# Optimization experiments

Hardware: AMD Instinct MI355X
Metric: run time of the kernel (lower is better)

The kernel has to match this reference:

```python
import jax, jax.numpy as jnp
import numpy as np

B, N, D = 4, 2048, 1024
H, A, Lv = 8, 128, 128   # heads, attention_dim (qk), linear_dim (v)
NUM_BLOCKS = 4
QKV_W = (2 * Lv + 2 * A) * H  # 4096
NEG = -1e9


def setup_inputs() -> dict:
    key = jax.random.key(0)
    ks = jax.random.split(key, 10)
    past_lengths = jax.random.randint(ks[0], (B,), 0, N)
    past_ids = jax.random.randint(ks[1], (B, N), 0, 10000)
    past_embeddings = jax.random.normal(ks[2], (B, N, D), dtype=jnp.float32)
    # per-block parameters, stacked on leading block axis (xavier-ish scale)
    qkv_w = jax.random.normal(ks[3], (NUM_BLOCKS, D, QKV_W), dtype=jnp.float32) * (1.0 / np.sqrt(D))
    qkv_b = jnp.zeros((NUM_BLOCKS, QKV_W), dtype=jnp.float32)
    out_w = jax.random.normal(ks[4], (NUM_BLOCKS, Lv * H, D), dtype=jnp.float32) * (1.0 / np.sqrt(Lv * H))
    out_b = jnp.zeros((NUM_BLOCKS, D), dtype=jnp.float32)
    ln_g = jnp.ones((NUM_BLOCKS, D), dtype=jnp.float32)
    ln_b = jnp.zeros((NUM_BLOCKS, D), dtype=jnp.float32)
    return {"past_lengths": past_lengths, "past_ids": past_ids,
            "past_embeddings": past_embeddings, "qkv_w": qkv_w, "qkv_b": qkv_b,
            "out_w": out_w, "out_b": out_b, "ln_g": ln_g, "ln_b": ln_b}


def _layer_norm(x, g, b, eps=1e-5):
    mu = jnp.mean(x, axis=-1, keepdims=True)
    var = jnp.mean(jnp.square(x - mu), axis=-1, keepdims=True)
    return (x - mu) * jax.lax.rsqrt(var + eps) * g + b


def _block(x, mask, qw, qb, ow, ob, g, b):
    xn = _layer_norm(x, g, b)
    qkv = (xn @ qw + qb).reshape(B, N, H, 2 * Lv + 2 * A)
    q = qkv[..., :A]              # [B,N,H,A]
    k = qkv[..., A:2 * A]         # [B,N,H,A]
    v = qkv[..., 2 * A:2 * A + Lv]  # [B,N,H,Lv]
    scores = jnp.einsum('bnha,bmha->bhnm', q, k) / np.sqrt(A)
    # original: masked_fill(-inf) -> silu -> /N -> softmax; we mask after the
    # silu transform with a large-negative logit so masked weights are ~0
    logits = jnp.where(mask[:, None, :, :], jax.nn.silu(scores) / N, NEG)
    w = jax.nn.softmax(logits, axis=-1)
    attn = jnp.einsum('bhnm,bmhl->bnhl', w, v).reshape(B, N, H * Lv)
    return x + attn @ ow + ob


def reference(past_lengths, past_ids, past_embeddings, qkv_w, qkv_b, out_w, out_b, ln_g, ln_b):
    valid = past_ids != 0                                   # [B,N]
    causal = jnp.triu(jnp.ones((N, N), dtype=bool), k=1)     # faithful to buffer (triu, diag=1)
    mask = causal[None] & valid[:, None, :] & valid[:, :, None]  # [B,N,N]
    x = past_embeddings
    for i in range(NUM_BLOCKS):
        x = _block(x, mask, qkv_w[i], qkv_b[i], out_w[i], out_b[i], ln_g[i], ln_b[i])
    return x
```

## Files before the change

### kernel.cpp

```cpp
#include <hip/hip_runtime.h>

typedef __bf16 bf16_t;
typedef __bf16 bf16x8 __attribute__((ext_vector_type(8)));
typedef __bf16 bf16x4 __attribute__((ext_vector_type(4)));
typedef float f32x4 __attribute__((ext_vector_type(4)));
typedef unsigned int u32x4 __attribute__((ext_vector_type(4)));

#define B_ 4
#define N_ 2048
#define D_ 1024
#define H_ 8
#define NB_ 4
#define M_ (B_*N_)
#define QN_ 3072
#define QKN_ 2048

__device__ __forceinline__ void async_copy16(const void* gsrc, void* ldst) {
    __builtin_amdgcn_global_load_lds(
        (const __attribute__((address_space(1))) void*)gsrc,
        (__attribute__((address_space(3))) void*)ldst, 16, 0, 0);
}

static constexpr size_t WT_OFF  = 0;
static constexpr size_t WT_SZ   = (size_t)NB_*QN_*D_*2;
static constexpr size_t OWT_OFF = WT_OFF + WT_SZ;
static constexpr size_t OWT_SZ  = (size_t)NB_*D_*D_*2;
static constexpr size_t XN_OFF  = OWT_OFF + OWT_SZ;
static constexpr size_t XN_SZ   = (size_t)M_*D_*2;
static constexpr size_t QK_OFF  = XN_OFF + XN_SZ;
static constexpr size_t QK_SZ   = (size_t)M_*QKN_*2;
static constexpr size_t VT_OFF  = QK_OFF + QK_SZ;
static constexpr size_t VT_SZ   = (size_t)32*128*N_*2;
static constexpr size_t ATT_OFF = VT_OFF + VT_SZ;
static constexpr size_t ATT_SZ  = (size_t)M_*D_*2;
static constexpr size_t QBR_OFF = ATT_OFF + ATT_SZ;
static constexpr size_t QBR_SZ  = (size_t)NB_*QN_*4;
static constexpr size_t VS_OFF  = QBR_OFF + QBR_SZ;
static constexpr size_t VS_SZ   = (size_t)32*128*4;
static constexpr size_t MASK_OFF = VS_OFF + VS_SZ;

__global__ __launch_bounds__(256) void repack_qkvw(const float* __restrict__ qw, bf16_t* __restrict__ wt)
{
    __shared__ float tile[64][65];
    const int nb = blockIdx.z;
    const int j0 = blockIdx.x * 64, d0 = blockIdx.y * 64;
    const int tx = threadIdx.x, ty = threadIdx.y;
    const float* src = qw + (size_t)nb * D_ * 4096;
    const int jj = j0 + tx;
    const int sel = jj >> 10, rr = jj & 1023, hh = rr >> 7, aa = rr & 127;
    const int orig = hh * 512 + sel * 128 + aa;
#pragma unroll
    for (int it = 0; it < 16; ++it) {
        int dr = it * 4 + ty;
        tile[dr][tx] = src[(size_t)(d0 + dr) * 4096 + orig];
    }
    __syncthreads();
    bf16_t* dst = wt + (size_t)nb * QN_ * D_;
#pragma unroll
    for (int it = 0; it < 16; ++it) {
        int jr = it * 4 + ty;
        dst[(size_t)(j0 + jr) * D_ + d0 + tx] = (bf16_t)tile[tx][jr];
    }
}

__global__ __launch_bounds__(256) void repack_outw(const float* __restrict__ ow, bf16_t* __restrict__ owt)
{
    __shared__ float tile[64][65];
    const int nb = blockIdx.z;
    const int j0 = blockIdx.x * 64, d0 = blockIdx.y * 64;
    const int tx = threadIdx.x, ty = threadIdx.y;
    const float* src = ow + (size_t)nb * D_ * D_;
#pragma unroll
    for (int it = 0; it < 16; ++it) {
        int dr = it * 4 + ty;
        tile[dr][tx] = src[(size_t)(d0 + dr) * D_ + j0 + tx];
    }
    __syncthreads();
    bf16_t* dst = owt + (size_t)nb * D_ * D_;
#pragma unroll
    for (int it = 0; it < 16; ++it) {
        int jr = it * 4 + ty;
        dst[(size_t)(j0 + jr) * D_ + d0 + tx] = (bf16_t)tile[tx][jr];
    }
}

__global__ __launch_bounds__(256) void repack_qb(const float* __restrict__ qb, float* __restrict__ qbr)
{
    int idx = blockIdx.x * 256 + threadIdx.x;
    int nb = idx / QN_, jj = idx % QN_;
    int sel = jj >> 10, rr = jj & 1023, hh = rr >> 7, aa = rr & 127;
    qbr[idx] = qb[nb * 4096 + hh * 512 + sel * 128 + aa];
}

__global__ __launch_bounds__(256) void mask_kernel(const int* __restrict__ past_ids, unsigned short* __restrict__ maskA)
{
    const int idx = blockIdx.x * 256 + threadIdx.x;
    const int b = idx >> 11, P = idx & 2047;
    const int k = P & 31;
    const int m = (P & ~31) | (((k >> 2) & 1) << 4) | (((k >> 3) & 3) << 2) | (k & 3);
    maskA[idx] = past_ids[b * N_ + m] != 0 ? 0xFFFFu : 0u;
}

__global__ __launch_bounds__(256) void ln_kernel(const float* __restrict__ x, const float* __restrict__ g,
                                                 const float* __restrict__ bb, bf16_t* __restrict__ xn)
{
    const int row = blockIdx.x, tid = threadIdx.x;
    const float4 v = ((const float4*)(x + (size_t)row * D_))[tid];
    float s = v.x + v.y + v.z + v.w;
    float q = v.x * v.x + v.y * v.y + v.z * v.z + v.w * v.w;
#pragma unroll
    for (int d = 32; d >= 1; d >>= 1) { s += __shfl_xor(s, d); q += __shfl_xor(q, d); }
    __shared__ float ls[4], lq[4];
    if ((tid & 63) == 0) { ls[tid >> 6] = s; lq[tid >> 6] = q; }
    __syncthreads();
    s = ls[0] + ls[1] + ls[2] + ls[3];
    q = lq[0] + lq[1] + lq[2] + lq[3];
    const float mean = s * (1.f / 1024.f);
    const float var  = q * (1.f / 1024.f) - mean * mean;
    const float inv  = rsqrtf(var + 1e-5f);
    const float4 gg = ((const float4*)g)[tid];
    const float4 bv = ((const float4*)bb)[tid];
    bf16x4 o;
    o[0] = (bf16_t)((v.x - mean) * inv * gg.x + bv.x);
    o[1] = (bf16_t)((v.y - mean) * inv * gg.y + bv.y);
    o[2] = (bf16_t)((v.z - mean) * inv * gg.z + bv.z);
    o[3] = (bf16_t)((v.w - mean) * inv * gg.w + bv.w);
    *(bf16x4*)(xn + (size_t)row * D_ + tid * 4) = o;
}

__global__ __launch_bounds__(512, 2) void gemm_qkv(const bf16_t* __restrict__ Am, const bf16_t* __restrict__ Bt,
                                                   const float* __restrict__ bias,
                                                   bf16_t* __restrict__ outQK, bf16_t* __restrict__ vtOut)
{
    __shared__ bf16_t As[4 * 8192];
    __shared__ bf16_t Bs[4 * 6144];
    const int tid = threadIdx.x;
    const int lane = tid & 63, wave = tid >> 6;
    const int wr = wave >> 2, wc = wave & 3;
    const int quad = lane >> 4, l15 = lane & 15;
    const int swz = quad ^ ((l15 >> 1) & 3);
    const int slane8 = ((lane & 3) ^ ((lane >> 3) & 3)) * 8;
    const int lrow = lane >> 2;
    const int m0 = blockIdx.y * 256, n0 = blockIdx.x * 192;
    const int Kn = D_;
    const bool w4 = (wave < 4);

    const int ch = wave * 2;
    const int bch0 = w4 ? 2 * wave : 4 + wave;
    const int bch1 = w4 ? 2 * wave + 1 : bch0;
    const bf16_t* gA0 = Am + (size_t)(m0 + ch * 16 + lrow) * Kn + slane8;
    const bf16_t* gA1 = gA0 + (size_t)16 * Kn;
    const bf16_t* gB0 = Bt + (size_t)(n0 + bch0 * 16 + lrow) * Kn + slane8;
    const bf16_t* gB1 = Bt + (size_t)(n0 + bch1 * 16 + lrow) * Kn + slane8;
    bf16_t* const dA0 = &As[ch * 512 + lane * 8];
    bf16_t* const dA1 = &As[(ch + 1) * 512 + lane * 8];
    bf16_t* const dB0 = &Bs[bch0 * 512 + lane * 8];
    bf16_t* const dB1 = &Bs[bch1 * 512 + lane * 8];

    auto STAGE = [&](int slot) {
        async_copy16(gA0, dA0 + slot * 8192);
        async_copy16(gA1, dA1 + slot * 8192);
        async_copy16(gB0, dB0 + slot * 6144);
        if (w4) async_copy16(gB1, dB1 + slot * 6144);
        gA0 += 32; gA1 += 32; gB0 += 32; gB1 += 32;
    };

    f32x4 acc[8][3] = {};
    const int NT = Kn >> 5;

    STAGE(0); STAGE(1); STAGE(2);
    if (w4) asm volatile("s_waitcnt vmcnt(8)" ::: "memory");
    else    asm volatile("s_waitcnt vmcnt(6)" ::: "memory");
    __builtin_amdgcn_s_barrier();

    const int aoff = wr * 4096 + l15 * 32 + swz * 8;
    const int boff = wc * 1536 + l15 * 32 + swz * 8;

    for (int t = 0; t < NT; ++t) {
        const int ring = t & 3;
        const bf16_t* ra = &As[ring * 8192 + aoff];
        const bf16_t* rb = &Bs[ring * 6144 + boff];
        bf16x8 af[8], bfv[3];
#pragma unroll
        for (int j = 0; j < 3; ++j) bfv[j] = *(const bf16x8*)(rb + j * 512);
#pragma unroll
        for (int i = 0; i < 8; ++i) af[i] = *(const bf16x8*)(ra + i * 512);
        if (t + 3 < NT) STAGE((t + 3) & 3);
        __builtin_amdgcn_s_setprio(1);
#pragma unroll
        for (int i = 0; i < 8; ++i)
#pragma unroll
            for (int j = 0; j < 3; ++j)
                acc[i][j] = __builtin_amdgcn_mfma_f32_16x16x32_bf16(af[i], bfv[j], acc[i][j], 0, 0, 0);
        __builtin_amdgcn_s_setprio(0);
        if (t + 3 < NT) {
            if (w4) asm volatile("s_waitcnt vmcnt(8)" ::: "memory");
            else    asm volatile("s_waitcnt vmcnt(6)" ::: "memory");
        } else if (t + 2 < NT) {
            if (w4) asm volatile("s_waitcnt vmcnt(4)" ::: "memory");
            else    asm volatile("s_waitcnt vmcnt(3)" ::: "memory");
        } else if (t + 1 < NT) {
            asm volatile("s_waitcnt vmcnt(0)" ::: "memory");
        }
        __builtin_amdgcn_s_barrier();
    }

#pragma unroll
    for (int i = 0; i < 8; ++i) {
        const int rowg = m0 + wr * 128 + i * 16 + quad * 4;
        const int bb2 = rowg >> 11, mloc = rowg & 2047;
        const int mperm = (mloc & ~31) | (((mloc >> 2) & 3) << 3) | (((mloc >> 4) & 1) << 2);
#pragma unroll
        for (int j = 0; j < 3; ++j) {
            const int colg = n0 + wc * 48 + j * 16 + l15;
            const float bv = bias[colg];
            if (colg >= 2048) {
                const int hh = (colg - 2048) >> 7, ll = (colg - 2048) & 127;
                bf16x4 sv;
#pragma unroll
                for (int r = 0; r < 4; ++r) sv[r] = (bf16_t)(acc[i][j][r] + bv);
                *(bf16x4*)(vtOut + ((size_t)(bb2 * 8 + hh) * 128 + ll) * (size_t)N_ + mperm) = sv;
            } else {
                const float qs = (colg < 1024) ? 0.08838834764831845f : 1.f;
#pragma unroll
                for (int r = 0; r < 4; ++r)
                    outQK[(size_t)(rowg + r) * QKN_ + colg] = (bf16_t)((acc[i][j][r] + bv) * qs);
            }
        }
    }
}

template<bool RESID>
__global__ __launch_bounds__(512, 2) void gemm256(const bf16_t* __restrict__ Am, const bf16_t* __restrict__ Bt,
                                                  const float* __restrict__ bias, float* __restrict__ resid_out,
                                                  bf16_t* __restrict__ outH, bf16_t* __restrict__ vtOut,
                                                  int Kn, int Nn, int vSplit)
{
    __shared__ bf16_t As[4 * 256 * 32];
    __shared__ bf16_t Bs[4 * 128 * 32];
    const int tid = threadIdx.x;
    const int lane = tid & 63, wave = tid >> 6;
    const int wr = wave >> 2, wc = wave & 3;
    const int quad = lane >> 4, l15 = lane & 15;
    const int swz = quad ^ ((l15 >> 1) & 3);
    const int slane8 = ((lane & 3) ^ ((lane >> 3) & 3)) * 8;
    const int lrow = lane >> 2;
    const int m0 = blockIdx.y * 256, n0 = blockIdx.x * 128;

    const int chA0 = wave * 2, chA1 = chA0 + 1;
    const bf16_t* gA0 = Am + (size_t)(m0 + chA0 * 16 + lrow) * Kn + slane8;
    const bf16_t* gA1 = Am + (size_t)(m0 + chA1 * 16 + lrow) * Kn + slane8;
    const bf16_t* gB  = Bt + (size_t)(n0 + wave * 16 + lrow) * Kn + slane8;
    bf16_t* const dA0 = &As[chA0 * 512];
    bf16_t* const dA1 = &As[chA1 * 512];
    bf16_t* const dB  = &Bs[wave * 512];

    auto STAGE = [&](int slot) {
        async_copy16(gA0, dA0 + slot * 8192);
        async_copy16(gA1, dA1 + slot * 8192);
        async_copy16(gB,  dB  + slot * 4096);
        gA0 += 32; gA1 += 32; gB += 32;
    };

    f32x4 acc[8][2] = {};
    const int NT = Kn >> 5;

    STAGE(0); STAGE(1); STAGE(2);
    asm volatile("s_waitcnt vmcnt(6)" ::: "memory");
    __builtin_amdgcn_s_barrier();

    const int aoff = (wr * 128 + l15) * 32 + swz * 8;
    const int boff = (wc * 32  + l15) * 32 + swz * 8;

    for (int t = 0; t < NT; ++t) {
        const int ring = t & 3;
        const bf16_t* ra = &As[ring * 8192 + aoff];
        const bf16_t* rb = &Bs[ring * 4096 + boff];
        bf16x8 af[8], bfv[2];
#pragma unroll
        for (int i = 0; i < 8; ++i) af[i] = *(const bf16x8*)(ra + i * 512);
#pragma unroll
        for (int j = 0; j < 2; ++j) bfv[j] = *(const bf16x8*)(rb + j * 512);
        if (t + 3 < NT) STAGE((t + 3) & 3);
        __builtin_amdgcn_s_barrier();
        asm volatile("s_waitcnt lgkmcnt(0)" ::: "memory");
        __builtin_amdgcn_s_setprio(1);
#pragma unroll
        for (int i = 0; i < 8; ++i)
#pragma unroll
            for (int j = 0; j < 2; ++j)
                acc[i][j] = __builtin_amdgcn_mfma_f32_16x16x32_bf16(af[i], bfv[j], acc[i][j], 0, 0, 0);
        __builtin_amdgcn_s_setprio(0);
        if (t + 3 < NT)      asm volatile("s_waitcnt vmcnt(6)" ::: "memory");
        else if (t + 2 < NT) asm volatile("s_waitcnt vmcnt(3)" ::: "memory");
        else if (t + 1 < NT) asm volatile("s_waitcnt vmcnt(0)" ::: "memory");
        __builtin_amdgcn_s_barrier();
    }

    if (!RESID && n0 >= vSplit) {
#pragma unroll
        for (int i = 0; i < 8; ++i) {
            const int rowg = m0 + wr * 128 + i * 16 + quad * 4;
            const int bb2 = rowg >> 11, mloc = rowg & 2047;
            const int mperm = (mloc & ~31) | (((mloc >> 2) & 3) << 3) | (((mloc >> 4) & 1) << 2);
#pragma unroll
            for (int j = 0; j < 2; ++j) {
                const int colg = n0 + wc * 32 + j * 16 + l15;
                const int hh = (colg - 2048) >> 7, ll = (colg - 2048) & 127;
                const float bv = bias[colg];
                bf16x4 sv;
#pragma unroll
                for (int r = 0; r < 4; ++r) sv[r] = (bf16_t)(acc[i][j][r] + bv);
                *(bf16x4*)(vtOut + ((size_t)(bb2 * 8 + hh) * 128 + ll) * (size_t)N_ + mperm) = sv;
            }
        }
        return;
    }
#pragma unroll
    for (int i = 0; i < 8; ++i) {
#pragma unroll
        for (int j = 0; j < 2; ++j) {
            const int colg = n0 + wc * 32 + j * 16 + l15;
            const float bv = bias[colg];
#pragma unroll
            for (int r = 0; r < 4; ++r) {
                const int rowg = m0 + wr * 128 + i * 16 + quad * 4 + r;
                const size_t off = (size_t)rowg * Nn + colg;
                const float v = acc[i][j][r] + bv;
                if (RESID) resid_out[off] += v;
                else       outH[off] = (bf16_t)v;
            }
        }
    }
}

__global__ __launch_bounds__(256) void vsum_kernel(const bf16_t* __restrict__ vt, float* __restrict__ vs)
{
    const int gid = blockIdx.x * 4 + (threadIdx.x >> 6);
    const int lane = threadIdx.x & 63;
    const bf16_t* p = vt + (size_t)gid * N_ + lane * 8;
    float s = 0.f;
#pragma unroll
    for (int c = 0; c < 4; ++c) {
        bf16x8 v = *(const bf16x8*)(p + c * 512);
#pragma unroll
        for (int u = 0; u < 8; ++u) s += (float)v[u];
    }
#pragma unroll
    for (int d = 32; d >= 1; d >>= 1) s += __shfl_xor(s, d);
    if (lane == 0) vs[gid] = s;
}

template<bool CAUSAL>
__device__ __forceinline__ void attn_tile(
    int m0, int m0n, int n0, int b, int h,
    const bf16_t* __restrict__ qk, const bf16_t* __restrict__ vtb,
    const unsigned short* __restrict__ maskB,
    bf16_t* Ks, bf16_t* Vs,
    const bf16x8 (&qf)[2][4], bf16x8 onesf,
    f32x4 (&oacc)[2][8], f32x4 (&dacc)[2])
{
    const int tid = threadIdx.x, lane = tid & 63, wave = tid >> 6;
    const int quad = lane >> 4, l15 = lane & 15;
    const int swz = quad ^ ((l15 >> 1) & 3);
    const int slane8 = ((lane & 3) ^ ((lane >> 3) & 3)) * 8;
    const int lrow = lane >> 2;
    const float invN = 1.f / 2048.f;

#pragma unroll
    for (int s = 0; s < 8; ++s) {
        const int kkc = s & 3, rg = (s >> 2) + wave * 2;
        async_copy16(vtb + (size_t)(rg * 16 + lrow) * N_ + m0 + kkc * 32 + slane8,
                     &Vs[kkc * 4096 + rg * 512 + lane * 8]);
    }
    bf16x8 mAf[4];
#pragma unroll
    for (int kk = 0; kk < 4; ++kk)
        mAf[kk] = *(const bf16x8*)(maskB + m0 + kk * 32 + quad * 8);

    f32x4 sacc[2][8] = {};
    __builtin_amdgcn_s_setprio(1);
#pragma unroll
    for (int kk = 0; kk < 4; ++kk) {
#pragma unroll
        for (int j = 0; j < 8; ++j) {
            bf16x8 kf = *(const bf16x8*)&Ks[kk * 4096 + (j * 16 + l15) * 32 + swz * 8];
            sacc[0][j] = __builtin_amdgcn_mfma_f32_16x16x32_bf16(kf, qf[0][kk], sacc[0][j], 0, 0, 0);
            sacc[1][j] = __builtin_amdgcn_mfma_f32_16x16x32_bf16(kf, qf[1][kk], sacc[1][j], 0, 0, 0);
        }
    }
    __builtin_amdgcn_s_setprio(0);

    bf16x8 pf[2][4];
#pragma unroll
    for (int kk = 0; kk < 4; ++kk) {
#pragma unroll
        for (int s = 0; s < 2; ++s) {
            const int j = kk * 2 + s;
#pragma unroll
            for (int nb = 0; nb < 2; ++nb) {
#pragma unroll
                for (int r = 0; r < 4; ++r) {
                    const float sv = sacc[nb][j][r];
                    const float xc = __builtin_amdgcn_fmed3f(sv, -4.f, 4.f);
                    float sg = __builtin_fmaf(xc, 0.25f * invN, 0.5f * invN);
                    sg = __builtin_fmaf(-(xc * (0.03125f * invN)), fabsf(xc), sg);
                    float e = __builtin_fmaf(sv, sg, 1.f);
                    if (CAUSAL) {
                        const int dmn = (m0 + j * 16 + quad * 4 + r) - (n0 + wave * 32 + nb * 16 + l15);
                        e = (dmn > 0) ? e : 0.f;
                    }
                    pf[nb][kk][s * 4 + r] = (bf16_t)e;
                }
            }
        }
        *(u32x4*)&pf[0][kk] = *(u32x4*)&pf[0][kk] & *(const u32x4*)&mAf[kk];
        *(u32x4*)&pf[1][kk] = *(u32x4*)&pf[1][kk] & *(const u32x4*)&mAf[kk];
    }

    __syncthreads();

    if (m0n < N_) {
        const size_t baseq = (size_t)b * N_ * QKN_;
#pragma unroll
        for (int s = 0; s < 8; ++s) {
            const int kkc = s & 3, rg = (s >> 2) + wave * 2;
            async_copy16(qk + baseq + (size_t)(m0n + rg * 16 + lrow) * QKN_ + 1024 + h * 128 + kkc * 32 + slane8,
                         &Ks[kkc * 4096 + rg * 512 + lane * 8]);
        }
    }

    __builtin_amdgcn_s_setprio(1);
#pragma unroll
    for (int kk = 0; kk < 4; ++kk) {
        dacc[0] = __builtin_amdgcn_mfma_f32_16x16x32_bf16(pf[0][kk], onesf, dacc[0], 0, 0, 0);
        dacc[1] = __builtin_amdgcn_mfma_f32_16x16x32_bf16(pf[1][kk], onesf, dacc[1], 0, 0, 0);
#pragma unroll
        for (int j = 0; j < 8; ++j) {
            bf16x8 vf = *(const bf16x8*)&Vs[kk * 4096 + (j * 16 + l15) * 32 + swz * 8];
            oacc[0][j] = __builtin_amdgcn_mfma_f32_16x16x32_bf16(pf[0][kk], vf, oacc[0][j], 0, 0, 0);
            oacc[1][j] = __builtin_amdgcn_mfma_f32_16x16x32_bf16(pf[1][kk], vf, oacc[1][j], 0, 0, 0);
        }
    }
    __builtin_amdgcn_s_setprio(0);
    __syncthreads();
}

__global__ __launch_bounds__(256, 2) void attn_kernel(const bf16_t* __restrict__ qk, const bf16_t* __restrict__ vt,
                                                      const int* __restrict__ past_ids, const float* __restrict__ vsum,
                                                      const unsigned short* __restrict__ maskA,
                                                      bf16_t* __restrict__ att)
{
    __shared__ bf16_t Ks[4 * 128 * 32];
    __shared__ bf16_t Vs[4 * 128 * 32];

    const int bx = blockIdx.x;
    const int bh = bx & 31, g = bx >> 5;
    const int t = (g < 8) ? g : 23 - g;
    const int b = bh >> 3, h = bh & 7;
    const int n0 = t << 7;
    const int tid = threadIdx.x, lane = tid & 63, wave = tid >> 6;
    const int quad = lane >> 4, l15 = lane & 15;
    const int slane8 = ((lane & 3) ^ ((lane >> 3) & 3)) * 8;
    const int lrow = lane >> 2;
    const bf16_t* vtb = vt + (size_t)bh * 128 * N_;
    const unsigned short* maskB = maskA + b * N_;
    const float invN = 1.f / 2048.f;

    bf16x8 qf[2][4];
#pragma unroll
    for (int nb = 0; nb < 2; ++nb) {
        const bf16_t* gq = qk + (size_t)b * N_ * QKN_ + (size_t)(n0 + wave * 32 + nb * 16 + l15) * QKN_ + h * 128 + quad * 8;
#pragma unroll
        for (int kk = 0; kk < 4; ++kk) qf[nb][kk] = *(const bf16x8*)(gq + kk * 32);
    }
    const float vnf0 = past_ids[b * N_ + n0 + wave * 32 + l15] != 0 ? 1.f : 0.f;
    const float vnf1 = past_ids[b * N_ + n0 + wave * 32 + 16 + l15] != 0 ? 1.f : 0.f;
    bf16x8 onesf;
#pragma unroll
    for (int i = 0; i < 8; ++i) onesf[i] = (bf16_t)1.f;

    {
        const size_t baseq = (size_t)b * N_ * QKN_;
#pragma unroll
        for (int s = 0; s < 8; ++s) {
            const int kkc = s & 3, rg = (s >> 2) + wave * 2;
            async_copy16(qk + baseq + (size_t)(n0 + rg * 16 + lrow) * QKN_ + 1024 + h * 128 + kkc * 32 + slane8,
                         &Ks[kkc * 4096 + rg * 512 + lane * 8]);
        }
    }
    __syncthreads();

    f32x4 oacc[2][8] = {};
    f32x4 dacc[2] = {};

    attn_tile<true>(n0, n0 + 128, n0, b, h, qk, vtb, maskB, Ks, Vs, qf, onesf, oacc, dacc);
    for (int m0 = n0 + 128; m0 < N_; m0 += 128)
        attn_tile<false>(m0, m0 + 128, n0, b, h, qk, vtb, maskB, Ks, Vs, qf, onesf, oacc, dacc);

    float vsr[8];
#pragma unroll
    for (int j = 0; j < 8; ++j) vsr[j] = vsum[bh * 128 + j * 16 + l15];
#pragma unroll
    for (int nb = 0; nb < 2; ++nb) {
        const float vn = nb ? vnf1 : vnf0;
#pragma unroll
        for (int r = 0; r < 4; ++r) {
            const float dn = dacc[nb][r];
            const bool uni = (vn == 0.f) || !(dn > 0.f);
            const float rc = uni ? 0.f : __builtin_amdgcn_rcpf(dn);
            const int gn = n0 + wave * 32 + nb * 16 + quad * 4 + r;
#pragma unroll
            for (int j = 0; j < 8; ++j) {
                const float ov = uni ? (vsr[j] * invN) : (oacc[nb][j][r] * rc);
                att[(size_t)(b * N_ + gn) * 1024 + h * 128 + j * 16 + l15] = (bf16_t)ov;
            }
        }
    }
}

extern "C" void kernel_launch(void* const* d_in, const int* in_sizes, int n_in,
                              void* d_out, int out_size, void* d_ws, size_t ws_size,
                              hipStream_t stream) {
    (void)in_sizes; (void)n_in; (void)out_size; (void)ws_size;
    const int*   past_ids = (const int*)d_in[1];
    const float* past_emb = (const float*)d_in[2];
    const float* qkv_w    = (const float*)d_in[3];
    const float* qkv_b    = (const float*)d_in[4];
    const float* out_w    = (const float*)d_in[5];
    const float* out_b    = (const float*)d_in[6];
    const float* ln_g     = (const float*)d_in[7];
    const float* ln_b     = (const float*)d_in[8];

    float* x = (float*)d_out;
    char* ws = (char*)d_ws;
    bf16_t* WT  = (bf16_t*)(ws + WT_OFF);
    bf16_t* OWT = (bf16_t*)(ws + OWT_OFF);
    bf16_t* XN  = (bf16_t*)(ws + XN_OFF);
    bf16_t* QK  = (bf16_t*)(ws + QK_OFF);
    bf16_t* VT  = (bf16_t*)(ws + VT_OFF);
    bf16_t* ATT = (bf16_t*)(ws + ATT_OFF);
    float*  QBR = (float*)(ws + QBR_OFF);
    float*  VS  = (float*)(ws + VS_OFF);
    unsigned short* MASKA = (unsigned short*)(ws + MASK_OFF);

    hipMemcpyAsync(x, past_emb, (size_t)M_ * D_ * sizeof(float), hipMemcpyDeviceToDevice, stream);
    repack_qkvw<<<dim3(48, 16, NB_), dim3(64, 4), 0, stream>>>(qkv_w, WT);
    repack_outw<<<dim3(16, 16, NB_), dim3(64, 4), 0, stream>>>(out_w, OWT);
    repack_qb<<<48, 256, 0, stream>>>(qkv_b, QBR);
    mask_kernel<<<32, 256, 0, stream>>>(past_ids, MASKA);

    for (int layer = 0; layer < NB_; ++layer) {
        ln_kernel<<<M_, 256, 0, stream>>>(x, ln_g + layer * D_, ln_b + layer * D_, XN);
        gemm_qkv<<<dim3(QN_ / 192, M_ / 256), 512, 0, stream>>>(
            XN, WT + (size_t)layer * QN_ * D_, QBR + layer * QN_, QK, VT);
        vsum_kernel<<<1024, 256, 0, stream>>>(VT, VS);
        attn_kernel<<<512, 256, 0, stream>>>(QK, VT, past_ids, VS, MASKA, ATT);
        gemm256<true><<<dim3(D_ / 128, M_ / 256), 512, 0, stream>>>(
            ATT, OWT + (size_t)layer * D_ * D_, out_b + layer * D_, x, nullptr, nullptr, D_, D_, 1 << 30);
    }
}
```

Baseline: 868.6 us.

## Fuse V column sums into QKV GEMM epilogue and drop the initial residual copy

The per-head V row sums are now accumulated in the QKV GEMM epilogue with wave shuffles and atomicAdd into per-layer buffers that the mask kernel zeroes, so the separate vsum kernel is removed. The up-front device-to-device copy of the embeddings is gone: layer 0 reads past_emb directly and the output GEMM writes resid_in plus the projection instead of accumulating in place. The output GEMM also drops a barrier and an explicit LDS wait in its main loop, and changes how it computes its LDS staging addresses. The aim is to save one kernel launch per layer and one 32 MB copy, at the cost of float atomics whose summation order is nondeterministic.

```diff
diff --git a/kernel.cpp b/kernel.cpp
--- a/kernel.cpp
+++ b/kernel.cpp
@@ -36,7 +36,7 @@
 static constexpr size_t QBR_OFF = ATT_OFF + ATT_SZ;
 static constexpr size_t QBR_SZ  = (size_t)NB_*QN_*4;
 static constexpr size_t VS_OFF  = QBR_OFF + QBR_SZ;
-static constexpr size_t VS_SZ   = (size_t)32*128*4;
+static constexpr size_t VS_SZ   = (size_t)NB_*32*128*4;
 static constexpr size_t MASK_OFF = VS_OFF + VS_SZ;
 
 __global__ __launch_bounds__(256) void repack_qkvw(const float* __restrict__ qw, bf16_t* __restrict__ wt)
@@ -92,9 +92,11 @@
     qbr[idx] = qb[nb * 4096 + hh * 512 + sel * 128 + aa];
 }
 
-__global__ __launch_bounds__(256) void mask_kernel(const int* __restrict__ past_ids, unsigned short* __restrict__ maskA)
+__global__ __launch_bounds__(256) void mask_kernel(const int* __restrict__ past_ids, unsigned short* __restrict__ maskA,
+                                                   float* __restrict__ vsl)
 {
     const int idx = blockIdx.x * 256 + threadIdx.x;
+    vsl[idx] = 0.f; vsl[idx + 8192] = 0.f;
     const int b = idx >> 11, P = idx & 2047;
     const int k = P & 31;
     const int m = (P & ~31) | (((k >> 2) & 1) << 4) | (((k >> 3) & 3) << 2) | (k & 3);
@@ -130,7 +132,8 @@
 
 __global__ __launch_bounds__(512, 2) void gemm_qkv(const bf16_t* __restrict__ Am, const bf16_t* __restrict__ Bt,
                                                    const float* __restrict__ bias,
-                                                   bf16_t* __restrict__ outQK, bf16_t* __restrict__ vtOut)
+                                                   bf16_t* __restrict__ outQK, bf16_t* __restrict__ vtOut,
+                                                   float* __restrict__ vsOut)
 {
     __shared__ bf16_t As[4 * 8192];
     __shared__ bf16_t Bs[4 * 6144];
@@ -205,23 +208,32 @@
         __builtin_amdgcn_s_barrier();
     }
 
-#pragma unroll
-    for (int i = 0; i < 8; ++i) {
-        const int rowg = m0 + wr * 128 + i * 16 + quad * 4;
-        const int bb2 = rowg >> 11, mloc = rowg & 2047;
-        const int mperm = (mloc & ~31) | (((mloc >> 2) & 3) << 3) | (((mloc >> 4) & 1) << 2);
-#pragma unroll
-        for (int j = 0; j < 3; ++j) {
-            const int colg = n0 + wc * 48 + j * 16 + l15;
-            const float bv = bias[colg];
-            if (colg >= 2048) {
-                const int hh = (colg - 2048) >> 7, ll = (colg - 2048) & 127;
+    const int bb2 = m0 >> 11;
+#pragma unroll
+    for (int j = 0; j < 3; ++j) {
+        const int colg = n0 + wc * 48 + j * 16 + l15;
+        const float bv = bias[colg];
+        if (colg >= 2048) {
+            const int hh = (colg - 2048) >> 7, ll = (colg - 2048) & 127;
+            float ps = 32.f * bv;
+#pragma unroll
+            for (int i = 0; i < 8; ++i) {
+                const int rowg = m0 + wr * 128 + i * 16 + quad * 4;
+                const int mloc = rowg & 2047;
+                const int mperm = (mloc & ~31) | (((mloc >> 2) & 3) << 3) | (((mloc >> 4) & 1) << 2);
                 bf16x4 sv;
 #pragma unroll
-                for (int r = 0; r < 4; ++r) sv[r] = (bf16_t)(acc[i][j][r] + bv);
+                for (int r = 0; r < 4; ++r) { sv[r] = (bf16_t)(acc[i][j][r] + bv); ps += acc[i][j][r]; }
                 *(bf16x4*)(vtOut + ((size_t)(bb2 * 8 + hh) * 128 + ll) * (size_t)N_ + mperm) = sv;
-            } else {
-                const float qs = (colg < 1024) ? 0.08838834764831845f : 1.f;
+            }
+            ps += __shfl_xor(ps, 16);
+            ps += __shfl_xor(ps, 32);
+            if (quad == 0) atomicAdd(&vsOut[(size_t)(bb2 * 8 + hh) * 128 + ll], ps);
+        } else {
+            const float qs = (colg < 1024) ? 0.08838834764831845f : 1.f;
+#pragma unroll
+            for (int i = 0; i < 8; ++i) {
+                const int rowg = m0 + wr * 128 + i * 16 + quad * 4;
 #pragma unroll
                 for (int r = 0; r < 4; ++r)
                     outQK[(size_t)(rowg + r) * QKN_ + colg] = (bf16_t)((acc[i][j][r] + bv) * qs);
@@ -230,11 +242,9 @@
     }
 }
 
-template<bool RESID>
-__global__ __launch_bounds__(512, 2) void gemm256(const bf16_t* __restrict__ Am, const bf16_t* __restrict__ Bt,
-                                                  const float* __restrict__ bias, float* __restrict__ resid_out,
-                                                  bf16_t* __restrict__ outH, bf16_t* __restrict__ vtOut,
-                                                  int Kn, int Nn, int vSplit)
+__global__ __launch_bounds__(512, 2) void gemm_out(const bf16_t* __restrict__ Am, const bf16_t* __restrict__ Bt,
+                                                   const float* __restrict__ bias,
+                                                   const float* __restrict__ resid_in, float* __restrict__ resid_out)
 {
     __shared__ bf16_t As[4 * 256 * 32];
     __shared__ bf16_t Bs[4 * 128 * 32];
@@ -246,14 +256,15 @@
     const int slane8 = ((lane & 3) ^ ((lane >> 3) & 3)) * 8;
     const int lrow = lane >> 2;
     const int m0 = blockIdx.y * 256, n0 = blockIdx.x * 128;
+    const int Kn = D_;
 
     const int chA0 = wave * 2, chA1 = chA0 + 1;
     const bf16_t* gA0 = Am + (size_t)(m0 + chA0 * 16 + lrow) * Kn + slane8;
     const bf16_t* gA1 = Am + (size_t)(m0 + chA1 * 16 + lrow) * Kn + slane8;
     const bf16_t* gB  = Bt + (size_t)(n0 + wave * 16 + lrow) * Kn + slane8;
-    bf16_t* const dA0 = &As[chA0 * 512];
-    bf16_t* const dA1 = &As[chA1 * 512];
-    bf16_t* const dB  = &Bs[wave * 512];
+    bf16_t* const dA0 = &As[chA0 * 512 + lane * 8];
+    bf16_t* const dA1 = &As[chA1 * 512 + lane * 8];
+    bf16_t* const dB  = &Bs[wave * 512 + lane * 8];
 
     auto STAGE = [&](int slot) {
         async_copy16(gA0, dA0 + slot * 8192);
@@ -278,12 +289,10 @@
         const bf16_t* rb = &Bs[ring * 4096 + boff];
         bf16x8 af[8], bfv[2];
 #pragma unroll
+        for (int j = 0; j < 2; ++j) bfv[j] = *(const bf16x8*)(rb + j * 512);
+#pragma unroll
         for (int i = 0; i < 8; ++i) af[i] = *(const bf16x8*)(ra + i * 512);
-#pragma unroll
-        for (int j = 0; j < 2; ++j) bfv[j] = *(const bf16x8*)(rb + j * 512);
         if (t + 3 < NT) STAGE((t + 3) & 3);
-        __builtin_amdgcn_s_barrier();
-        asm volatile("s_waitcnt lgkmcnt(0)" ::: "memory");
         __builtin_amdgcn_s_setprio(1);
 #pragma unroll
         for (int i = 0; i < 8; ++i)
@@ -297,25 +306,6 @@
         __builtin_amdgcn_s_barrier();
     }
 
-    if (!RESID && n0 >= vSplit) {
-#pragma unroll
-        for (int i = 0; i < 8; ++i) {
-            const int rowg = m0 + wr * 128 + i * 16 + quad * 4;
-            const int bb2 = rowg >> 11, mloc = rowg & 2047;
-            const int mperm = (mloc & ~31) | (((mloc >> 2) & 3) << 3) | (((mloc >> 4) & 1) << 2);
-#pragma unroll
-            for (int j = 0; j < 2; ++j) {
-                const int colg = n0 + wc * 32 + j * 16 + l15;
-                const int hh = (colg - 2048) >> 7, ll = (colg - 2048) & 127;
-                const float bv = bias[colg];
-                bf16x4 sv;
-#pragma unroll
-                for (int r = 0; r < 4; ++r) sv[r] = (bf16_t)(acc[i][j][r] + bv);
-                *(bf16x4*)(vtOut + ((size_t)(bb2 * 8 + hh) * 128 + ll) * (size_t)N_ + mperm) = sv;
-            }
-        }
-        return;
-    }
 #pragma unroll
     for (int i = 0; i < 8; ++i) {
 #pragma unroll
@@ -325,30 +315,11 @@
 #pragma unroll
             for (int r = 0; r < 4; ++r) {
                 const int rowg = m0 + wr * 128 + i * 16 + quad * 4 + r;
-                const size_t off = (size_t)rowg * Nn + colg;
-                const float v = acc[i][j][r] + bv;
-                if (RESID) resid_out[off] += v;
-                else       outH[off] = (bf16_t)v;
+                const size_t off = (size_t)rowg * D_ + colg;
+                resid_out[off] = resid_in[off] + acc[i][j][r] + bv;
             }
         }
     }
-}
-
-__global__ __launch_bounds__(256) void vsum_kernel(const bf16_t* __restrict__ vt, float* __restrict__ vs)
-{
-    const int gid = blockIdx.x * 4 + (threadIdx.x >> 6);
-    const int lane = threadIdx.x & 63;
-    const bf16_t* p = vt + (size_t)gid * N_ + lane * 8;
-    float s = 0.f;
-#pragma unroll
-    for (int c = 0; c < 4; ++c) {
-        bf16x8 v = *(const bf16x8*)(p + c * 512);
-#pragma unroll
-        for (int u = 0; u < 8; ++u) s += (float)v[u];
-    }
-#pragma unroll
-    for (int d = 32; d >= 1; d >>= 1) s += __shfl_xor(s, d);
-    if (lane == 0) vs[gid] = s;
 }
 
 template<bool CAUSAL>
@@ -541,22 +512,21 @@
     bf16_t* VT  = (bf16_t*)(ws + VT_OFF);
     bf16_t* ATT = (bf16_t*)(ws + ATT_OFF);
     float*  QBR = (float*)(ws + QBR_OFF);
-    float*  VS  = (float*)(ws + VS_OFF);
+    float*  VSL = (float*)(ws + VS_OFF);
     unsigned short* MASKA = (unsigned short*)(ws + MASK_OFF);
 
-    hipMemcpyAsync(x, past_emb, (size_t)M_ * D_ * sizeof(float), hipMemcpyDeviceToDevice, stream);
     repack_qkvw<<<dim3(48, 16, NB_), dim3(64, 4), 0, stream>>>(qkv_w, WT);
     repack_outw<<<dim3(16, 16, NB_), dim3(64, 4), 0, stream>>>(out_w, OWT);
     repack_qb<<<48, 256, 0, stream>>>(qkv_b, QBR);
-    mask_kernel<<<32, 256, 0, stream>>>(past_ids, MASKA);
+    mask_kernel<<<32, 256, 0, stream>>>(past_ids, MASKA, VSL);
 
     for (int layer = 0; layer < NB_; ++layer) {
-        ln_kernel<<<M_, 256, 0, stream>>>(x, ln_g + layer * D_, ln_b + layer * D_, XN);
+        const float* xin = (layer == 0) ? past_emb : x;
+        ln_kernel<<<M_, 256, 0, stream>>>(xin, ln_g + layer * D_, ln_b + layer * D_, XN);
         gemm_qkv<<<dim3(QN_ / 192, M_ / 256), 512, 0, stream>>>(
-            XN, WT + (size_t)layer * QN_ * D_, QBR + layer * QN_, QK, VT);
-        vsum_kernel<<<1024, 256, 0, stream>>>(VT, VS);
-        attn_kernel<<<512, 256, 0, stream>>>(QK, VT, past_ids, VS, MASKA, ATT);
-        gemm256<true><<<dim3(D_ / 128, M_ / 256), 512, 0, stream>>>(
-            ATT, OWT + (size_t)layer * D_ * D_, out_b + layer * D_, x, nullptr, nullptr, D_, D_, 1 << 30);
-    }
-}
+            XN, WT + (size_t)layer * QN_ * D_, QBR + layer * QN_, QK, VT, VSL + layer * 4096);
+        attn_kernel<<<512, 256, 0, stream>>>(QK, VT, past_ids, VSL + layer * 4096, MASKA, ATT);
+        gemm_out<<<dim3(D_ / 128, M_ / 256), 512, 0, stream>>>(
+            ATT, OWT + (size_t)layer * D_ * D_, out_b + layer * D_, xin, x);
+    }
+}
```

Result: faster. 828.7 us (-4.6%).
